# Performance work log

Measured on AMD Instinct MI355X. Metric: run time of the kernel, lower is better.

The kernel has to match this reference:

```python
import jax, jax.numpy as jnp
import numpy as np

B, L = 4096, 200
USER_COUNT, ITEM_COUNT, CATE_COUNT = 100000, 100000, 1000
USER_DIM, ITEM_DIM, CATE_DIM = 128, 64, 64
BN_EPS = 1e-5


def setup_inputs() -> dict:
    key = jax.random.key(0)
    ks = jax.random.split(key, 16)
    # ragged history: valid prefix of `length` items (ids >= 1), zero-padded tail
    length = jax.random.randint(ks[3], (B,), 1, L + 1)
    hist_raw = jax.random.randint(ks[2], (B, L), 1, ITEM_COUNT)
    history = jnp.where(jnp.arange(L)[None, :] < length[:, None], hist_raw, 0)
    inp = {
        "user": jax.random.randint(ks[0], (B,), 0, USER_COUNT),
        "item": jax.random.randint(ks[1], (B,), 0, ITEM_COUNT),
        "history": history,
        "length": length,
        "cate_list": jax.random.randint(ks[4], (ITEM_COUNT,), 0, CATE_COUNT),
        "user_emb_W": jax.random.normal(ks[5], (USER_COUNT, USER_DIM), jnp.float32) * 0.05,
        "item_emb_W": jax.random.normal(ks[6], (ITEM_COUNT, ITEM_DIM), jnp.float32) * 0.05,
        "cate_emb_W": jax.random.normal(ks[7], (CATE_COUNT, CATE_DIM), jnp.float32) * 0.05,
        "bn_gamma": 1.0 + 0.1 * jax.random.normal(ks[8], (384,), jnp.float32),
        "bn_beta": 0.1 * jax.random.normal(ks[9], (384,), jnp.float32),
        "W1": jax.random.normal(ks[10], (200, 384), jnp.float32) * (1.0 / np.sqrt(384)),
        "b1": jnp.zeros((200,), jnp.float32),
        "a1": jnp.full((), 0.25, jnp.float32),
        "W2": jax.random.normal(ks[11], (80, 200), jnp.float32) * (1.0 / np.sqrt(200)),
        "b2": jnp.zeros((80,), jnp.float32),
        "a2": jnp.full((), 0.25, jnp.float32),
        "W3": jax.random.normal(ks[12], (2, 80), jnp.float32) * (1.0 / np.sqrt(80)),
        "b3": jnp.zeros((2,), jnp.float32),
    }
    return inp


def _prelu(x, a):
    return jnp.where(x >= 0, x, a * x)


def reference(user, item, history, length, cate_list,
              user_emb_W, item_emb_W, cate_emb_W, bn_gamma, bn_beta,
              W1, b1, a1, W2, b2, a2, W3, b3):
    u = user_emb_W[user]                                              # [B,128]
    it = jnp.concatenate([item_emb_W[item], cate_emb_W[cate_list[item]]], -1)  # [B,128]

    # Faithful replication of get_emb's loop semantics:
    # row b uses the prefix of `history[b]` up to (and incl.) the position
    # just before the first zero; a row whose first entry is 0 halts the
    # outer loop, zeroing that row and all following rows.
    nz = history != 0                                                 # [B,L]
    prefix = jnp.concatenate(
        [jnp.ones((history.shape[0], 1), bool),
         jnp.cumprod(nz[:, 1:].astype(jnp.int32), axis=1).astype(bool)], axis=1)
    row_active = jnp.cumprod(nz[:, 0].astype(jnp.int32)).astype(bool)  # outer break
    mask = prefix & row_active[:, None]                               # [B,L]

    he = jnp.concatenate([item_emb_W[history], cate_emb_W[cate_list[history]]], -1)  # [B,L,128]
    cnt = jnp.maximum(mask.sum(-1), 1).astype(he.dtype)               # [B]
    pooled = (he * mask[..., None].astype(he.dtype)).sum(1) / cnt[:, None]  # [B,128]

    x = jnp.concatenate([u, it, pooled], -1)                          # [B,384]
    # BatchNorm1d in training mode (batch stats, biased variance)
    mean = x.mean(0)
    var = x.var(0)
    x = (x - mean) * jax.lax.rsqrt(var + BN_EPS) * bn_gamma + bn_beta
    x = _prelu(x @ W1.T + b1, a1)
    x = _prelu(x @ W2.T + b2, a2)
    x = x @ W3.T + b3
    return jax.nn.softmax(x, axis=1)
```

## Files before the change

### kernel.cpp

```cpp
#include <hip/hip_runtime.h>
#include <hip/hip_bf16.h>

#define B_SZ 4096
#define L_SZ 200

typedef __bf16 bf16x8 __attribute__((ext_vector_type(8)));
typedef float  f32x4  __attribute__((ext_vector_type(4)));

static __device__ inline unsigned short bfbits(float f) {
    return __builtin_bit_cast(unsigned short, (__bf16)f);
}
static __device__ inline float bf2f(unsigned short u) {
    return __builtin_bit_cast(float, (unsigned int)u << 16);
}

#define NB_ICVT 6250
#define NB_CCVT 63
#define NB_WFR  48

__global__ __launch_bounds__(256) void k_pre(
    const float* __restrict__ item_W, const float* __restrict__ cate_W,
    const float* __restrict__ W1, const float* __restrict__ W2,
    const int* __restrict__ history,
    ushort* __restrict__ item_bf, ushort* __restrict__ cate_bf,
    ushort* __restrict__ W1f, ushort* __restrict__ W2f,
    int* __restrict__ first_bad, float* __restrict__ acc)
{
    const int bid = blockIdx.x, tid = threadIdx.x;
    if (bid < NB_ICVT) {
        int idx = bid * 256 + tid;
        float4 v = ((const float4*)item_W)[idx];
        ((ushort4*)item_bf)[idx] =
            make_ushort4(bfbits(v.x), bfbits(v.y), bfbits(v.z), bfbits(v.w));
    } else if (bid < NB_ICVT + NB_CCVT) {
        int idx = (bid - NB_ICVT) * 256 + tid;
        if (idx < 16000) {
            float4 v = ((const float4*)cate_W)[idx];
            ((ushort4*)cate_bf)[idx] =
                make_ushort4(bfbits(v.x), bfbits(v.y), bfbits(v.z), bfbits(v.w));
        }
    } else if (bid < NB_ICVT + NB_CCVT + NB_WFR) {
        const int chunk = (bid - NB_ICVT - NB_CCVT) * 4 + (tid >> 6);
        const int lane = tid & 63, nr = lane & 15, quad = lane >> 4;
        if (chunk < 191) {
            ushort v[8];
            if (chunk < 156) {
                const int oT = chunk / 12, kS = chunk % 12;
                const int o = oT * 16 + nr;
                #pragma unroll
                for (int j = 0; j < 8; ++j) {
                    int k = kS * 32 + quad * 8 + j;
                    v[j] = (o < 200) ? bfbits(W1[(size_t)o * 384 + k]) : (ushort)0;
                }
                ushort* dst = W1f + ((size_t)chunk * 64 + lane) * 8;
                *(ushort4*)(dst)     = make_ushort4(v[0], v[1], v[2], v[3]);
                *(ushort4*)(dst + 4) = make_ushort4(v[4], v[5], v[6], v[7]);
            } else {
                const int idx = chunk - 156;
                const int oT = idx / 7, kS = idx % 7;
                const int o = oT * 16 + nr;
                #pragma unroll
                for (int j = 0; j < 8; ++j) {
                    int k = kS * 32 + quad * 8 + j;
                    v[j] = (k < 200) ? bfbits(W2[(size_t)o * 200 + k]) : (ushort)0;
                }
                ushort* dst = W2f + ((size_t)idx * 64 + lane) * 8;
                *(ushort4*)(dst)     = make_ushort4(v[0], v[1], v[2], v[3]);
                *(ushort4*)(dst + 4) = make_ushort4(v[4], v[5], v[6], v[7]);
            }
        }
    } else {
        acc[tid] = 0.f; acc[256 + tid] = 0.f; acc[512 + tid] = 0.f;
        int m = B_SZ;
        for (int b = tid; b < B_SZ; b += 256)
            if (history[(size_t)b * L_SZ] == 0) m = min(m, b);
        __shared__ int red[256];
        red[tid] = m;
        __syncthreads();
        for (int s = 128; s > 0; s >>= 1) {
            if (tid < s) red[tid] = min(red[tid], red[tid + s]);
            __syncthreads();
        }
        if (tid == 0) first_bad[0] = red[0];
    }
}

__global__ __launch_bounds__(256) void k_pool(
    const int* __restrict__ user, const int* __restrict__ item,
    const int* __restrict__ history, const int* __restrict__ cate_list,
    const float* __restrict__ user_W, const float* __restrict__ item_W,
    const float* __restrict__ cate_W,
    const ushort* __restrict__ item_bf, const ushort* __restrict__ cate_bf,
    ushort* __restrict__ xb)
{
    const int b = blockIdx.x;
    const int tid = threadIdx.x;
    __shared__ int sh_item[L_SZ];
    __shared__ int sh_cid[L_SZ];
    __shared__ int s_fz;
    __shared__ __align__(16) float red[16][128];
    if (tid == 0) s_fz = L_SZ;
    __syncthreads();
    if (tid < L_SZ) {
        int h = history[(size_t)b * L_SZ + tid];
        sh_item[tid] = h;
        if (tid >= 1 && h == 0) atomicMin(&s_fz, tid);
        sh_cid[tid] = cate_list[h];
    }
    __syncthreads();
    const int valid = s_fz;
    const float inv_cnt = 1.0f / (float)max(valid, 1);

    const int p = tid >> 4, sub = (tid >> 3) & 1, q = tid & 7;
    const ushort* tab = sub ? cate_bf : item_bf;
    const int*    ids = sub ? sh_cid : sh_item;
    float a0 = 0.f, a1_ = 0.f, a2_ = 0.f, a3 = 0.f, a4 = 0.f, a5 = 0.f, a6 = 0.f, a7 = 0.f;
    int l = p;
    for (; l + 16 < valid; l += 32) {
        bf16x8 v0 = *(const bf16x8*)(tab + (size_t)ids[l] * 64 + q * 8);
        bf16x8 v1 = *(const bf16x8*)(tab + (size_t)ids[l + 16] * 64 + q * 8);
        a0 += (float)v0[0] + (float)v1[0]; a1_ += (float)v0[1] + (float)v1[1];
        a2_ += (float)v0[2] + (float)v1[2]; a3 += (float)v0[3] + (float)v1[3];
        a4 += (float)v0[4] + (float)v1[4]; a5 += (float)v0[5] + (float)v1[5];
        a6 += (float)v0[6] + (float)v1[6]; a7 += (float)v0[7] + (float)v1[7];
    }
    if (l < valid) {
        bf16x8 v0 = *(const bf16x8*)(tab + (size_t)ids[l] * 64 + q * 8);
        a0 += (float)v0[0]; a1_ += (float)v0[1]; a2_ += (float)v0[2]; a3 += (float)v0[3];
        a4 += (float)v0[4]; a5 += (float)v0[5]; a6 += (float)v0[6]; a7 += (float)v0[7];
    }
    float* rp = &red[p][sub * 64 + q * 8];
    *(float4*)(rp)     = make_float4(a0, a1_, a2_, a3);
    *(float4*)(rp + 4) = make_float4(a4, a5, a6, a7);
    __syncthreads();

    ushort* xrow = xb + (size_t)b * 384;
    if (tid < 128) {
        float s = 0.f;
        #pragma unroll
        for (int g = 0; g < 16; ++g) s += red[g][tid];
        xrow[256 + tid] = bfbits(s * inv_cnt);
        xrow[tid] = bfbits(user_W[(size_t)user[b] * 128 + tid]);
    } else if (tid < 192) {
        int f = tid - 128;
        xrow[128 + f] = bfbits(item_W[(size_t)item[b] * 64 + f]);
    } else {
        int f = tid - 192;
        xrow[192 + f] = bfbits(cate_W[(size_t)cate_list[item[b]] * 64 + f]);
    }
}

__global__ __launch_bounds__(384) void k_bnstats(const ushort* __restrict__ xb,
                                                 const int* __restrict__ first_bad,
                                                 float* __restrict__ acc) {
    const int f = threadIdx.x;
    const int r0 = blockIdx.x * 64;
    const int fb = first_bad[0];
    const bool pooled = (f >= 256);
    float s = 0.f, s2 = 0.f;
    for (int r = r0; r < r0 + 64; ++r) {
        float v = bf2f(xb[(size_t)r * 384 + f]);
        if (pooled && r >= fb) v = 0.f;
        s += v; s2 += v * v;
    }
    atomicAdd(&acc[f], s);
    atomicAdd(&acc[384 + f], s2);
}

__global__ __launch_bounds__(256) void k_l1(
    const ushort* __restrict__ xb, const float* __restrict__ accv,
    const float* __restrict__ gamma, const float* __restrict__ beta,
    const ushort* __restrict__ W1f, const float* __restrict__ b1,
    const float* __restrict__ a1p, const int* __restrict__ first_bad,
    ushort* __restrict__ h1b)
{
    __shared__ float As[384], Cs[384];
    const int tid = threadIdx.x;
    for (int f = tid; f < 384; f += 256) {
        const float inv_b = 1.0f / (float)B_SZ;
        float mean = accv[f] * inv_b;
        float var  = accv[384 + f] * inv_b - mean * mean;
        float a = gamma[f] * rsqrtf(var + 1e-5f);
        As[f] = a;
        Cs[f] = beta[f] - mean * a;
    }
    __syncthreads();

    const int lane = tid & 63, wv = tid >> 6;
    const int nr = lane & 15, quad = lane >> 4;
    const int wid = blockIdx.x * 4 + wv;
    const int mT = wid / 13, oT = wid - mT * 13;
    const int o = oT * 16 + nr;
    const float a1 = a1p[0];
    const int fb = first_bad[0];
    const bool badrow = (mT * 16 + nr) >= fb;

    float bias = (o < 200) ? b1[o] : 0.f;
    f32x4 acc = {bias, bias, bias, bias};
    const ushort* xrow = xb + (size_t)(mT * 16 + nr) * 384;

    #pragma unroll 2
    for (int kS = 0; kS < 8; ++kS) {
        const int kc = kS * 32 + quad * 8;
        bf16x8 a8 = *(const bf16x8*)(xrow + kc);
        float4 A0 = *(const float4*)&As[kc], A1 = *(const float4*)&As[kc + 4];
        float4 C0 = *(const float4*)&Cs[kc], C1 = *(const float4*)&Cs[kc + 4];
        bf16x8 w;
        w[0] = (__bf16)((float)a8[0] * A0.x + C0.x);
        w[1] = (__bf16)((float)a8[1] * A0.y + C0.y);
        w[2] = (__bf16)((float)a8[2] * A0.z + C0.z);
        w[3] = (__bf16)((float)a8[3] * A0.w + C0.w);
        w[4] = (__bf16)((float)a8[4] * A1.x + C1.x);
        w[5] = (__bf16)((float)a8[5] * A1.y + C1.y);
        w[6] = (__bf16)((float)a8[6] * A1.z + C1.z);
        w[7] = (__bf16)((float)a8[7] * A1.w + C1.w);
        bf16x8 bfr = *(const bf16x8*)(W1f + (((size_t)oT * 12 + kS) * 64 + lane) * 8);
        acc = __builtin_amdgcn_mfma_f32_16x16x32_bf16(w, bfr, acc, 0, 0, 0);
    }
    #pragma unroll 2
    for (int kS = 8; kS < 12; ++kS) {
        const int kc = kS * 32 + quad * 8;
        bf16x8 a8 = *(const bf16x8*)(xrow + kc);
        if (badrow) {
            #pragma unroll
            for (int j = 0; j < 8; ++j) a8[j] = (__bf16)0.f;
        }
        float4 A0 = *(const float4*)&As[kc], A1 = *(const float4*)&As[kc + 4];
        float4 C0 = *(const float4*)&Cs[kc], C1 = *(const float4*)&Cs[kc + 4];
        bf16x8 w;
        w[0] = (__bf16)((float)a8[0] * A0.x + C0.x);
        w[1] = (__bf16)((float)a8[1] * A0.y + C0.y);
        w[2] = (__bf16)((float)a8[2] * A0.z + C0.z);
        w[3] = (__bf16)((float)a8[3] * A0.w + C0.w);
        w[4] = (__bf16)((float)a8[4] * A1.x + C1.x);
        w[5] = (__bf16)((float)a8[5] * A1.y + C1.y);
        w[6] = (__bf16)((float)a8[6] * A1.z + C1.z);
        w[7] = (__bf16)((float)a8[7] * A1.w + C1.w);
        bf16x8 bfr = *(const bf16x8*)(W1f + (((size_t)oT * 12 + kS) * 64 + lane) * 8);
        acc = __builtin_amdgcn_mfma_f32_16x16x32_bf16(w, bfr, acc, 0, 0, 0);
    }

    #pragma unroll
    for (int r = 0; r < 4; ++r) {
        int row = mT * 16 + quad * 4 + r;
        float s = acc[r];
        s = (s >= 0.f) ? s : a1 * s;
        h1b[(size_t)row * 224 + o] = bfbits(s);
        if (oT == 12) h1b[(size_t)row * 224 + o + 16] = 0;
    }
}

__global__ __launch_bounds__(256) void k_l23(
    const ushort* __restrict__ h1b, const ushort* __restrict__ W2f,
    const float* __restrict__ b2, const float* __restrict__ a2p,
    const float* __restrict__ W3, const float* __restrict__ b3,
    float* __restrict__ out)
{
    const int tid = threadIdx.x;
    const int lane = tid & 63, wv = tid >> 6;
    const int nr = lane & 15, quad = lane >> 4;
    const int mT = blockIdx.x * 4 + wv;
    const float a2 = a2p[0];

    f32x4 acc[5];
    #pragma unroll
    for (int i = 0; i < 5; ++i) {
        float bb = b2[i * 16 + nr];
        acc[i] = (f32x4){bb, bb, bb, bb};
    }
    const ushort* hrow = h1b + (size_t)(mT * 16 + nr) * 224;
    for (int kS = 0; kS < 7; ++kS) {
        bf16x8 a8 = *(const bf16x8*)(hrow + kS * 32 + quad * 8);
        #pragma unroll
        for (int i = 0; i < 5; ++i) {
            bf16x8 bfr = *(const bf16x8*)(W2f + (((size_t)i * 7 + kS) * 64 + lane) * 8);
            acc[i] = __builtin_amdgcn_mfma_f32_16x16x32_bf16(a8, bfr, acc[i], 0, 0, 0);
        }
    }

    float w0[5], w1[5];
    #pragma unroll
    for (int i = 0; i < 5; ++i) {
        w0[i] = W3[i * 16 + nr];
        w1[i] = W3[80 + i * 16 + nr];
    }
    f32x4 p0 = {0.f, 0.f, 0.f, 0.f}, p1 = {0.f, 0.f, 0.f, 0.f};
    #pragma unroll
    for (int i = 0; i < 5; ++i) {
        #pragma unroll
        for (int r = 0; r < 4; ++r) {
            float s = acc[i][r];
            s = (s >= 0.f) ? s : a2 * s;
            p0[r] += s * w0[i];
            p1[r] += s * w1[i];
        }
    }
    #pragma unroll
    for (int m = 1; m < 16; m <<= 1) {
        #pragma unroll
        for (int r = 0; r < 4; ++r) {
            p0[r] += __shfl_xor(p0[r], m, 64);
            p1[r] += __shfl_xor(p1[r], m, 64);
        }
    }
    if (nr == 0) {
        float B0 = b3[0], B1 = b3[1];
        #pragma unroll
        for (int r = 0; r < 4; ++r) {
            float l0 = p0[r] + B0, l1 = p1[r] + B1;
            float mx = fmaxf(l0, l1);
            float e0 = expf(l0 - mx), e1 = expf(l1 - mx);
            float inv = 1.0f / (e0 + e1);
            int row = mT * 16 + quad * 4 + r;
            *(float2*)(out + (size_t)row * 2) = make_float2(e0 * inv, e1 * inv);
        }
    }
}

extern "C" void kernel_launch(void* const* d_in, const int* in_sizes, int n_in,
                              void* d_out, int out_size, void* d_ws, size_t ws_size,
                              hipStream_t stream) {
    const int*   user      = (const int*)  d_in[0];
    const int*   item      = (const int*)  d_in[1];
    const int*   history   = (const int*)  d_in[2];
    const int*   cate_list = (const int*)  d_in[4];
    const float* user_W    = (const float*)d_in[5];
    const float* item_W    = (const float*)d_in[6];
    const float* cate_W    = (const float*)d_in[7];
    const float* gamma     = (const float*)d_in[8];
    const float* beta      = (const float*)d_in[9];
    const float* W1        = (const float*)d_in[10];
    const float* b1        = (const float*)d_in[11];
    const float* a1        = (const float*)d_in[12];
    const float* W2        = (const float*)d_in[13];
    const float* b2        = (const float*)d_in[14];
    const float* a2        = (const float*)d_in[15];
    const float* W3        = (const float*)d_in[16];
    const float* b3        = (const float*)d_in[17];
    float* out = (float*)d_out;

    char* ws = (char*)d_ws;
    int*    first_bad = (int*)   ws;
    float*  acc       = (float*)(ws + 64);
    ushort* xb        = (ushort*)(ws + 3200);
    ushort* h1b       = (ushort*)(ws + 3148928);
    ushort* W1f       = (ushort*)(ws + 4983936);
    ushort* W2f       = (ushort*)(ws + 5143680);
    ushort* item_bf   = (ushort*)(ws + 5179520);
    ushort* cate_bf   = (ushort*)(ws + 17979520);

    hipLaunchKernelGGL(k_pre,     dim3(NB_ICVT + NB_CCVT + NB_WFR + 1), dim3(256), 0, stream,
                       item_W, cate_W, W1, W2, history,
                       item_bf, cate_bf, W1f, W2f, first_bad, acc);
    hipLaunchKernelGGL(k_pool,    dim3(B_SZ), dim3(256), 0, stream,
                       user, item, history, cate_list, user_W, item_W, cate_W,
                       item_bf, cate_bf, xb);
    hipLaunchKernelGGL(k_bnstats, dim3(64),   dim3(384), 0, stream, xb, first_bad, acc);
    hipLaunchKernelGGL(k_l1,      dim3(832),  dim3(256), 0, stream,
                       xb, acc, gamma, beta, W1f, b1, a1, first_bad, h1b);
    hipLaunchKernelGGL(k_l23,     dim3(64),   dim3(256), 0, stream,
                       h1b, W2f, b2, a2, W3, b3, out);
}
```

Before: 181.5 us.

## Fuse MLP layer 1 with layers 2-3 through shared memory per row tile

Merges the first MLP layer kernel and the layer2/layer3/softmax kernel into one kernel where each block owns a 16-row tile and keeps the layer-1 activations in LDS instead of writing them to global memory. This removes one kernel launch and the global round trip of the hidden activations. The grid shrinks from 832 to 256 blocks. Each wave now computes several output tiles and the final logits are reduced by 16 threads serially, so parallelism is lower and LDS plus barriers are added.

Result: slower. 193.4 us (+6.6%).

```diff
diff --git a/kernel.cpp b/kernel.cpp
--- a/kernel.cpp
+++ b/kernel.cpp
@@ -167,14 +167,20 @@
     atomicAdd(&acc[384 + f], s2);
 }
 
-__global__ __launch_bounds__(256) void k_l1(
+#define H1S 232
+
+__global__ __launch_bounds__(256) void k_l1l23(
     const ushort* __restrict__ xb, const float* __restrict__ accv,
     const float* __restrict__ gamma, const float* __restrict__ beta,
     const ushort* __restrict__ W1f, const float* __restrict__ b1,
     const float* __restrict__ a1p, const int* __restrict__ first_bad,
-    ushort* __restrict__ h1b)
+    const ushort* __restrict__ W2f, const float* __restrict__ b2,
+    const float* __restrict__ a2p, const float* __restrict__ W3,
+    const float* __restrict__ b3, float* __restrict__ out)
 {
     __shared__ float As[384], Cs[384];
+    __shared__ __align__(16) __bf16 h1L[16 * H1S];
+    __shared__ __align__(16) float h2s[16][84];
     const int tid = threadIdx.x;
     for (int f = tid; f < 384; f += 256) {
         const float inv_b = 1.0f / (float)B_SZ;
@@ -188,21 +194,30 @@
 
     const int lane = tid & 63, wv = tid >> 6;
     const int nr = lane & 15, quad = lane >> 4;
-    const int wid = blockIdx.x * 4 + wv;
-    const int mT = wid / 13, oT = wid - mT * 13;
-    const int o = oT * 16 + nr;
+    const int mT = blockIdx.x;
     const float a1 = a1p[0];
     const int fb = first_bad[0];
     const bool badrow = (mT * 16 + nr) >= fb;
-
-    float bias = (o < 200) ? b1[o] : 0.f;
-    f32x4 acc = {bias, bias, bias, bias};
     const ushort* xrow = xb + (size_t)(mT * 16 + nr) * 384;
 
-    #pragma unroll 2
-    for (int kS = 0; kS < 8; ++kS) {
+    f32x4 acc4[4] = {{0.f,0.f,0.f,0.f},{0.f,0.f,0.f,0.f},
+                     {0.f,0.f,0.f,0.f},{0.f,0.f,0.f,0.f}};
+    #pragma unroll
+    for (int i = 0; i < 4; ++i) {
+        int oT = wv + 4 * i;
+        if (oT < 13) {
+            int o = oT * 16 + nr;
+            float bias = (o < 200) ? b1[o] : 0.f;
+            acc4[i] = (f32x4){bias, bias, bias, bias};
+        }
+    }
+    for (int kS = 0; kS < 12; ++kS) {
         const int kc = kS * 32 + quad * 8;
         bf16x8 a8 = *(const bf16x8*)(xrow + kc);
+        if (kS >= 8 && badrow) {
+            #pragma unroll
+            for (int j = 0; j < 8; ++j) a8[j] = (__bf16)0.f;
+        }
         float4 A0 = *(const float4*)&As[kc], A1 = *(const float4*)&As[kc + 4];
         float4 C0 = *(const float4*)&Cs[kc], C1 = *(const float4*)&Cs[kc + 4];
         bf16x8 w;
@@ -214,106 +229,79 @@
         w[5] = (__bf16)((float)a8[5] * A1.y + C1.y);
         w[6] = (__bf16)((float)a8[6] * A1.z + C1.z);
         w[7] = (__bf16)((float)a8[7] * A1.w + C1.w);
-        bf16x8 bfr = *(const bf16x8*)(W1f + (((size_t)oT * 12 + kS) * 64 + lane) * 8);
-        acc = __builtin_amdgcn_mfma_f32_16x16x32_bf16(w, bfr, acc, 0, 0, 0);
-    }
-    #pragma unroll 2
-    for (int kS = 8; kS < 12; ++kS) {
-        const int kc = kS * 32 + quad * 8;
-        bf16x8 a8 = *(const bf16x8*)(xrow + kc);
-        if (badrow) {
+        #pragma unroll
+        for (int i = 0; i < 4; ++i) {
+            int oT = wv + 4 * i;
+            if (oT < 13) {
+                bf16x8 bfr = *(const bf16x8*)(W1f + (((size_t)oT * 12 + kS) * 64 + lane) * 8);
+                acc4[i] = __builtin_amdgcn_mfma_f32_16x16x32_bf16(w, bfr, acc4[i], 0, 0, 0);
+            }
+        }
+    }
+    #pragma unroll
+    for (int i = 0; i < 4; ++i) {
+        int oT = wv + 4 * i;
+        if (oT < 13) {
+            int o = oT * 16 + nr;
             #pragma unroll
-            for (int j = 0; j < 8; ++j) a8[j] = (__bf16)0.f;
-        }
-        float4 A0 = *(const float4*)&As[kc], A1 = *(const float4*)&As[kc + 4];
-        float4 C0 = *(const float4*)&Cs[kc], C1 = *(const float4*)&Cs[kc + 4];
-        bf16x8 w;
-        w[0] = (__bf16)((float)a8[0] * A0.x + C0.x);
-        w[1] = (__bf16)((float)a8[1] * A0.y + C0.y);
-        w[2] = (__bf16)((float)a8[2] * A0.z + C0.z);
-        w[3] = (__bf16)((float)a8[3] * A0.w + C0.w);
-        w[4] = (__bf16)((float)a8[4] * A1.x + C1.x);
-        w[5] = (__bf16)((float)a8[5] * A1.y + C1.y);
-        w[6] = (__bf16)((float)a8[6] * A1.z + C1.z);
-        w[7] = (__bf16)((float)a8[7] * A1.w + C1.w);
-        bf16x8 bfr = *(const bf16x8*)(W1f + (((size_t)oT * 12 + kS) * 64 + lane) * 8);
-        acc = __builtin_amdgcn_mfma_f32_16x16x32_bf16(w, bfr, acc, 0, 0, 0);
-    }
-
+            for (int r = 0; r < 4; ++r) {
+                float s = acc4[i][r];
+                s = (s >= 0.f) ? s : a1 * s;
+                h1L[(quad * 4 + r) * H1S + o] = (__bf16)s;
+                if (oT == 12) h1L[(quad * 4 + r) * H1S + o + 16] = (__bf16)0.f;
+            }
+        }
+    }
+    __syncthreads();
+
+    const float a2 = a2p[0];
+    f32x4 acc5[2] = {{0.f,0.f,0.f,0.f},{0.f,0.f,0.f,0.f}};
     #pragma unroll
-    for (int r = 0; r < 4; ++r) {
-        int row = mT * 16 + quad * 4 + r;
-        float s = acc[r];
-        s = (s >= 0.f) ? s : a1 * s;
-        h1b[(size_t)row * 224 + o] = bfbits(s);
-        if (oT == 12) h1b[(size_t)row * 224 + o + 16] = 0;
-    }
-}
-
-__global__ __launch_bounds__(256) void k_l23(
-    const ushort* __restrict__ h1b, const ushort* __restrict__ W2f,
-    const float* __restrict__ b2, const float* __restrict__ a2p,
-    const float* __restrict__ W3, const float* __restrict__ b3,
-    float* __restrict__ out)
-{
-    const int tid = threadIdx.x;
-    const int lane = tid & 63, wv = tid >> 6;
-    const int nr = lane & 15, quad = lane >> 4;
-    const int mT = blockIdx.x * 4 + wv;
-    const float a2 = a2p[0];
-
-    f32x4 acc[5];
+    for (int i = 0; i < 2; ++i) {
+        int oT = wv + 4 * i;
+        if (oT < 5) {
+            float bb = b2[oT * 16 + nr];
+            acc5[i] = (f32x4){bb, bb, bb, bb};
+        }
+    }
+    for (int kS = 0; kS < 7; ++kS) {
+        bf16x8 a8 = *(const bf16x8*)&h1L[nr * H1S + kS * 32 + quad * 8];
+        #pragma unroll
+        for (int i = 0; i < 2; ++i) {
+            int oT = wv + 4 * i;
+            if (oT < 5) {
+                bf16x8 bfr = *(const bf16x8*)(W2f + (((size_t)oT * 7 + kS) * 64 + lane) * 8);
+                acc5[i] = __builtin_amdgcn_mfma_f32_16x16x32_bf16(a8, bfr, acc5[i], 0, 0, 0);
+            }
+        }
+    }
     #pragma unroll
-    for (int i = 0; i < 5; ++i) {
-        float bb = b2[i * 16 + nr];
-        acc[i] = (f32x4){bb, bb, bb, bb};
-    }
-    const ushort* hrow = h1b + (size_t)(mT * 16 + nr) * 224;
-    for (int kS = 0; kS < 7; ++kS) {
-        bf16x8 a8 = *(const bf16x8*)(hrow + kS * 32 + quad * 8);
-        #pragma unroll
-        for (int i = 0; i < 5; ++i) {
-            bf16x8 bfr = *(const bf16x8*)(W2f + (((size_t)i * 7 + kS) * 64 + lane) * 8);
-            acc[i] = __builtin_amdgcn_mfma_f32_16x16x32_bf16(a8, bfr, acc[i], 0, 0, 0);
-        }
-    }
-
-    float w0[5], w1[5];
-    #pragma unroll
-    for (int i = 0; i < 5; ++i) {
-        w0[i] = W3[i * 16 + nr];
-        w1[i] = W3[80 + i * 16 + nr];
-    }
-    f32x4 p0 = {0.f, 0.f, 0.f, 0.f}, p1 = {0.f, 0.f, 0.f, 0.f};
-    #pragma unroll
-    for (int i = 0; i < 5; ++i) {
-        #pragma unroll
-        for (int r = 0; r < 4; ++r) {
-            float s = acc[i][r];
-            s = (s >= 0.f) ? s : a2 * s;
-            p0[r] += s * w0[i];
-            p1[r] += s * w1[i];
-        }
-    }
-    #pragma unroll
-    for (int m = 1; m < 16; m <<= 1) {
-        #pragma unroll
-        for (int r = 0; r < 4; ++r) {
-            p0[r] += __shfl_xor(p0[r], m, 64);
-            p1[r] += __shfl_xor(p1[r], m, 64);
-        }
-    }
-    if (nr == 0) {
-        float B0 = b3[0], B1 = b3[1];
-        #pragma unroll
-        for (int r = 0; r < 4; ++r) {
-            float l0 = p0[r] + B0, l1 = p1[r] + B1;
-            float mx = fmaxf(l0, l1);
-            float e0 = expf(l0 - mx), e1 = expf(l1 - mx);
-            float inv = 1.0f / (e0 + e1);
-            int row = mT * 16 + quad * 4 + r;
-            *(float2*)(out + (size_t)row * 2) = make_float2(e0 * inv, e1 * inv);
-        }
+    for (int i = 0; i < 2; ++i) {
+        int oT = wv + 4 * i;
+        if (oT < 5) {
+            int o = oT * 16 + nr;
+            #pragma unroll
+            for (int r = 0; r < 4; ++r) {
+                float s = acc5[i][r];
+                h2s[quad * 4 + r][o] = (s >= 0.f) ? s : a2 * s;
+            }
+        }
+    }
+    __syncthreads();
+
+    if (tid < 16) {
+        float l0 = b3[0], l1v = b3[1];
+        #pragma unroll 8
+        for (int f = 0; f < 80; ++f) {
+            float h = h2s[tid][f];
+            l0  += h * W3[f];
+            l1v += h * W3[80 + f];
+        }
+        float mx = fmaxf(l0, l1v);
+        float e0 = expf(l0 - mx), e1 = expf(l1v - mx);
+        float inv = 1.0f / (e0 + e1);
+        int row = mT * 16 + tid;
+        *(float2*)(out + (size_t)row * 2) = make_float2(e0 * inv, e1 * inv);
     }
 }
 
@@ -343,7 +331,6 @@
     int*    first_bad = (int*)   ws;
     float*  acc       = (float*)(ws + 64);
     ushort* xb        = (ushort*)(ws + 3200);
-    ushort* h1b       = (ushort*)(ws + 3148928);
     ushort* W1f       = (ushort*)(ws + 4983936);
     ushort* W2f       = (ushort*)(ws + 5143680);
     ushort* item_bf   = (ushort*)(ws + 5179520);
@@ -356,8 +343,7 @@
                        user, item, history, cate_list, user_W, item_W, cate_W,
                        item_bf, cate_bf, xb);
     hipLaunchKernelGGL(k_bnstats, dim3(64),   dim3(384), 0, stream, xb, first_bad, acc);
-    hipLaunchKernelGGL(k_l1,      dim3(832),  dim3(256), 0, stream,
-                       xb, acc, gamma, beta, W1f, b1, a1, first_bad, h1b);
-    hipLaunchKernelGGL(k_l23,     dim3(64),   dim3(256), 0, stream,
-                       h1b, W2f, b2, a2, W3, b3, out);
-}
+    hipLaunchKernelGGL(k_l1l23,   dim3(256),  dim3(256), 0, stream,
+                       xb, acc, gamma, beta, W1f, b1, a1, first_bad,
+                       W2f, b2, a2, W3, b3, out);
+}
```
